# Performance work log

Measured on AMD Instinct MI355X. Metric: run time of the kernel, lower is better.

## Reference

```python
import jax, jax.numpy as jnp
import numpy as np

B, C, H, W = 128, 512, 14, 14
P = 512  # num_parts (codebook size)


def setup_inputs() -> dict:
    key = jax.random.key(0)
    k1, k2, k3 = jax.random.split(key, 3)
    fm = jax.random.normal(k1, (B, C, H, W), dtype=jnp.float32)
    embedding = jax.random.normal(k2, (B, C), dtype=jnp.float32)
    # self.w = torch.randn(P, C).clamp_(min=0)
    w = jnp.maximum(jax.random.normal(k3, (P, C), dtype=jnp.float32), 0.0)
    w_ep_sum = w  # clone of w at init
    w_ep_num = jnp.ones((P,), dtype=jnp.float32)
    return {"fm": fm, "embedding": embedding, "w": w,
            "w_ep_sum": w_ep_sum, "w_ep_num": w_ep_num, "epoch": 5}


def reference(fm, embedding, w, w_ep_sum, w_ep_num, epoch):
    b, c, h, wd = fm.shape
    p = w.shape[0]
    # NCHW -> [B, HW, C]
    x = jnp.transpose(fm, (0, 2, 3, 1)).reshape(b, h * wd, c)
    xf = x.reshape(b * h * wd, c)
    dist = (jnp.sum(xf * xf, axis=1, keepdims=True)
            + jnp.sum(w * w, axis=1)
            - 2.0 * (xf @ w.T))                      # [B*HW, P]
    assign = jax.nn.softmax(-dist.reshape(b, h * wd, p), axis=-1)
    # hard threshold: zero out weak assignments
    assign = jnp.where(assign < 1.0 / p, 0.0, assign)  # [B, HW, P]
    assign_sum = assign.mean(axis=1)                    # [B, P]

    if epoch > 2:  # epoch is a static Python int
        # relu(einsum('bn,nc->bnc').mean(1)) == relu((assign_sum @ w) / P)
        cvec = jax.nn.relu((assign_sum @ w) / p)        # [B, C]
        embedding_cat = jnp.concatenate([embedding, cvec], axis=-1)
    else:
        embedding_cat = jnp.concatenate([embedding, jnp.zeros_like(embedding)], axis=-1)

    # collect_weight (no-grad EMA-style accumulate).
    # einsum('bmn,bmc->bmnc').sum(1).sum(0) == einsum('bmn,bmc->nc') -- avoids
    # materializing the [B,M,N,C] tensor the torch code builds.
    update_w = jnp.einsum('bmn,bmc->nc', assign, x)     # [P, C]
    assign_mean = jnp.sum(assign, axis=(0, 1))          # [P]
    upd = assign_mean > 1.0
    new_w_ep_sum = jnp.where(upd[:, None], w_ep_sum + update_w, w_ep_sum)
    new_w_ep_num = jnp.where(upd, w_ep_num + assign_mean, w_ep_num)
    return embedding_cat, new_w_ep_sum, new_w_ep_num
```

## Files before the change

### kernel.cpp

```cpp
#include <hip/hip_runtime.h>
#include <hip/hip_bf16.h>

#define Bn   128
#define Cn   512
#define HWn  196
#define Mn   25088
#define Pn   512
#define SPLITK2 32
#define KCH  1024

#define OFF_XT     0u
#define OFF_AT     8388608u
#define OFF_PART   16777216u
#define OFF_XM     16777216u
#define OFF_WF     25165824u
#define OFF_WNORM  25296896u
#define OFF_RAWP   25297408u
#define OFF_MEAN   25428480u

#define OUT_CAT  0u
#define OUT_WSUM 131072u
#define OUT_WNUM 393216u

using bf16x8 = __attribute__((ext_vector_type(8))) short;
using f16x8  = __attribute__((ext_vector_type(8))) _Float16;
using f32x4  = __attribute__((ext_vector_type(4))) float;

__device__ __forceinline__ unsigned short f2b(float f) {
    union { float f; unsigned u; } x; x.f = f;
    unsigned r = x.u + 0x7fffu + ((x.u >> 16) & 1u);
    return (unsigned short)(r >> 16);
}

__global__ __launch_bounds__(64) void k_wnorm(const float* __restrict__ w,
                                              float* __restrict__ wn,
                                              _Float16* __restrict__ wf) {
    int n = blockIdx.x, l = threadIdx.x;
    const float* p = w + (size_t)n * Cn + l * 8;
    float4 a = *(const float4*)p;
    float4 b = *(const float4*)(p + 4);
    float s = a.x*a.x + a.y*a.y + a.z*a.z + a.w*a.w
            + b.x*b.x + b.y*b.y + b.z*b.z + b.w*b.w;
    alignas(16) _Float16 h[8];
    h[0]=(_Float16)a.x; h[1]=(_Float16)a.y; h[2]=(_Float16)a.z; h[3]=(_Float16)a.w;
    h[4]=(_Float16)b.x; h[5]=(_Float16)b.y; h[6]=(_Float16)b.z; h[7]=(_Float16)b.w;
    *(float4*)(wf + (size_t)(n >> 4) * 8192u + (size_t)(l >> 2) * 512
                 + (n & 15) * 32 + (l & 3) * 8) = *(const float4*)h;
    #pragma unroll
    for (int o = 32; o > 0; o >>= 1) s += __shfl_down(s, o);
    if (l == 0) wn[n] = s;
}

__global__ __launch_bounds__(512) void k_prep2(const float* __restrict__ fm,
                                               _Float16* __restrict__ xm,
                                               unsigned short* __restrict__ xt) {
    __shared__ _Float16 tile[64][200];
    int b = blockIdx.x;
    int cg = blockIdx.y * 64;
    int t = threadIdx.x;
    for (int i = t; i < 64 * 49; i += 512) {
        int cl = i / 49, h4 = i - cl * 49;
        float4 v = *(const float4*)(fm + ((size_t)(b * Cn + cg + cl) * HWn) + h4 * 4);
        tile[cl][h4*4+0] = (_Float16)v.x;
        tile[cl][h4*4+1] = (_Float16)v.y;
        tile[cl][h4*4+2] = (_Float16)v.z;
        tile[cl][h4*4+3] = (_Float16)v.w;
    }
    __syncthreads();
    for (int i = t; i < HWn * 8; i += 512) {
        int hw = i >> 3, seg = i & 7;
        alignas(16) _Float16 h[8];
        #pragma unroll
        for (int j = 0; j < 8; ++j) h[j] = tile[seg * 8 + j][hw];
        *(float4*)(xm + (size_t)(b * HWn + hw) * Cn + cg + seg * 8) = *(const float4*)h;
    }
    for (int i = t; i < 64 * 4 * 16; i += 512) {
        int cl = i >> 6, rem = i & 63;
        int q = rem >> 4, j4 = rem & 15;
        ushort4 o;
        if (j4 < 12) {
            o.x = f2b((float)tile[cl][q*49 + j4*4 + 0]);
            o.y = f2b((float)tile[cl][q*49 + j4*4 + 1]);
            o.z = f2b((float)tile[cl][q*49 + j4*4 + 2]);
            o.w = f2b((float)tile[cl][q*49 + j4*4 + 3]);
        } else if (j4 == 12) {
            o.x = f2b((float)tile[cl][q*49 + 48]);
            o.y = 0; o.z = 0; o.w = 0;
        } else {
            o.x = 0; o.y = 0; o.z = 0; o.w = 0;
        }
        int c = cg + cl;
        int T = c >> 4;
        int seg = b * 8 + q * 2 + (j4 >> 3);
        int k = (j4 & 7) * 4;
        *(ushort4*)(xt + (size_t)T * 524288u + (size_t)seg * 512 + (c & 15) * 32 + k) = o;
    }
}

__global__ __launch_bounds__(512) void k_post(const _Float16* __restrict__ xm,
                                              const _Float16* __restrict__ wf,
                                              const float* __restrict__ wnorm,
                                              unsigned short* __restrict__ at,
                                              float* __restrict__ rawp) {
    __shared__ _Float16 As[113][520];
    __shared__ float red[2][64][4];
    __shared__ float colp[2][512];
    const int bid = blockIdx.x;
    const int b = bid >> 1, half = bid & 1;
    const int tid = threadIdx.x;
    const int wave = tid >> 6, lane = tid & 63;
    const int mq = wave >> 2, nq = wave & 3;
    const int rl = lane & 15, rq = lane >> 4;
    const int kb = rq * 8;
    const int m0 = b * 196 + half * 98;
    const int n0 = nq * 128;

    for (int i = tid; i < 113 * 64; i += 512) {
        int row = i >> 6, kc = (i & 63) * 8;
        *(f16x8*)&As[row][kc] = *(const f16x8*)(xm + (size_t)(m0 + row) * Cn + kc);
    }
    __syncthreads();

    const _Float16* wtb = wf + (size_t)(nq * 8) * 8192u + rl * 32 + kb;

    f32x4 acc[4][8] = {};
    for (int seg = 0; seg < 16; ++seg) {
        f16x8 a[4], bb[8];
        #pragma unroll
        for (int f = 0; f < 4; ++f)
            a[f] = *(const f16x8*)&As[mq * 49 + f * 16 + rl][seg * 32 + kb];
        #pragma unroll
        for (int g = 0; g < 8; ++g)
            bb[g] = *(const f16x8*)(wtb + (size_t)g * 8192u + seg * 512);
        #pragma unroll
        for (int f = 0; f < 4; ++f)
            #pragma unroll
            for (int g = 0; g < 8; ++g)
                acc[f][g] = __builtin_amdgcn_mfma_f32_16x16x32_f16(a[f], bb[g], acc[f][g], 0, 0, 0);
    }
    float wn[8];
    #pragma unroll
    for (int g = 0; g < 8; ++g) wn[g] = wnorm[n0 + g * 16 + rl];
    #pragma unroll
    for (int f = 0; f < 4; ++f)
        #pragma unroll
        for (int g = 0; g < 8; ++g)
            #pragma unroll
            for (int r = 0; r < 4; ++r)
                acc[f][g][r] = 2.0f * acc[f][g][r] - wn[g];
    float mx[4][4];
    #pragma unroll
    for (int f = 0; f < 4; ++f)
        #pragma unroll
        for (int r = 0; r < 4; ++r) {
            float m_ = acc[f][0][r];
            #pragma unroll
            for (int g = 1; g < 8; ++g) m_ = fmaxf(m_, acc[f][g][r]);
            #pragma unroll
            for (int o = 8; o >= 1; o >>= 1) m_ = fmaxf(m_, __shfl_xor(m_, o));
            mx[f][r] = m_;
        }
    if (rl == 0)
        #pragma unroll
        for (int f = 0; f < 4; ++f)
            #pragma unroll
            for (int r = 0; r < 4; ++r)
                red[mq][f * 16 + rq * 4 + r][nq] = mx[f][r];
    __syncthreads();
    float rmax[4][4];
    #pragma unroll
    for (int f = 0; f < 4; ++f)
        #pragma unroll
        for (int r = 0; r < 4; ++r) {
            float* q = red[mq][f * 16 + rq * 4 + r];
            rmax[f][r] = fmaxf(fmaxf(q[0], q[1]), fmaxf(q[2], q[3]));
        }
    float sm[4][4];
    #pragma unroll
    for (int f = 0; f < 4; ++f)
        #pragma unroll
        for (int r = 0; r < 4; ++r) {
            float s_ = 0.f;
            #pragma unroll
            for (int g = 0; g < 8; ++g) {
                float p = __expf(acc[f][g][r] - rmax[f][r]);
                acc[f][g][r] = p;
                s_ += p;
            }
            #pragma unroll
            for (int o = 8; o >= 1; o >>= 1) s_ += __shfl_xor(s_, o);
            sm[f][r] = s_;
        }
    __syncthreads();
    if (rl == 0)
        #pragma unroll
        for (int f = 0; f < 4; ++f)
            #pragma unroll
            for (int r = 0; r < 4; ++r)
                red[mq][f * 16 + rq * 4 + r][nq] = sm[f][r];
    __syncthreads();
    const float invP = 1.0f / 512.0f;
    #pragma unroll
    for (int f = 0; f < 4; ++f)
        #pragma unroll
        for (int r = 0; r < 4; ++r) {
            float* q = red[mq][f * 16 + rq * 4 + r];
            float inv = 1.0f / (q[0] + q[1] + q[2] + q[3]);
            #pragma unroll
            for (int g = 0; g < 8; ++g) {
                float a = acc[f][g][r] * inv;
                acc[f][g][r] = (a < invP) ? 0.0f : a;
            }
        }
    float cs[8] = {};
    #pragma unroll
    for (int g = 0; g < 8; ++g) {
        #pragma unroll
        for (int f = 0; f < 4; ++f)
            #pragma unroll
            for (int r = 0; r < 4; ++r)
                if (f * 16 + rq * 4 + r < 49) cs[g] += acc[f][g][r];
        cs[g] += __shfl_xor(cs[g], 16);
        cs[g] += __shfl_xor(cs[g], 32);
    }
    if (rq == 0)
        #pragma unroll
        for (int g = 0; g < 8; ++g) colp[mq][n0 + g * 16 + rl] = cs[g];
    __syncthreads();
    if (tid < 512) rawp[(size_t)bid * 512 + tid] = colp[0][tid] + colp[1][tid];
    const int mb = b * 256 + (half * 2 + mq) * 64;
    const int segbase = mb >> 5;
    #pragma unroll
    for (int f = 0; f < 4; ++f) {
        const int mloc = f * 16 + rq * 4;
        const int seg = segbase + (mloc >> 5);
        const int k = mloc & 31;
        #pragma unroll
        for (int g = 0; g < 8; ++g) {
            ushort4 o;
            o.x = (mloc + 0 < 49) ? f2b(acc[f][g][0]) : (unsigned short)0;
            o.y = (mloc + 1 < 49) ? f2b(acc[f][g][1]) : (unsigned short)0;
            o.z = (mloc + 2 < 49) ? f2b(acc[f][g][2]) : (unsigned short)0;
            o.w = (mloc + 3 < 49) ? f2b(acc[f][g][3]) : (unsigned short)0;
            const int T = nq * 8 + g;
            *(ushort4*)(at + (size_t)T * 524288u + (size_t)seg * 512 + rl * 32 + k) = o;
        }
    }
}

__global__ __launch_bounds__(256) void k_reduce(const float* __restrict__ rawp,
                                                const float* __restrict__ wnum,
                                                float* __restrict__ mean,
                                                float* __restrict__ outnum) {
    int n = blockIdx.x * 256 + threadIdx.x;
    float s = 0.f;
    for (int r = 0; r < 256; ++r) s += rawp[(size_t)r * Pn + n];
    mean[n] = s;
    outnum[n] = wnum[n] + (s > 1.0f ? s : 0.0f);
}

__global__ __launch_bounds__(256) void k_cvec(const float* __restrict__ rawp,
                                              const float* __restrict__ w,
                                              const float* __restrict__ emb,
                                              const int* __restrict__ epoch,
                                              float* __restrict__ out) {
    __shared__ float srow[512];
    int b = blockIdx.x, t = threadIdx.x;
    srow[t]       = rawp[(size_t)(2*b) * Pn + t]       + rawp[(size_t)(2*b+1) * Pn + t];
    srow[t + 256] = rawp[(size_t)(2*b) * Pn + t + 256] + rawp[(size_t)(2*b+1) * Pn + t + 256];
    __syncthreads();
    float a0 = 0.f, a1 = 0.f;
    for (int p = 0; p < Pn; ++p) {
        float ap = srow[p];
        a0 = fmaf(ap, w[(size_t)p * Cn + t], a0);
        a1 = fmaf(ap, w[(size_t)p * Cn + t + 256], a1);
    }
    const float sc = 1.0f / (196.0f * 512.0f);
    int ep = epoch[0];
    float c0 = (ep > 2) ? fmaxf(a0, 0.f) * sc : 0.f;
    float c1 = (ep > 2) ? fmaxf(a1, 0.f) * sc : 0.f;
    out[(size_t)b * 1024 + t]             = emb[(size_t)b * Cn + t];
    out[(size_t)b * 1024 + t + 256]       = emb[(size_t)b * Cn + t + 256];
    out[(size_t)b * 1024 + 512 + t]       = c0;
    out[(size_t)b * 1024 + 512 + t + 256] = c1;
}

__global__ __launch_bounds__(256) void k_upw_mfma(const unsigned short* __restrict__ at,
                                                  const unsigned short* __restrict__ xt,
                                                  float* __restrict__ part) {
    const int id = blockIdx.x;
    const int sp = id & 31;
    const int m  = id >> 5;
    const int tid = threadIdx.x;
    const int wave = tid >> 6, lane = tid & 63;
    const int wn = wave >> 1, wc = wave & 1;
    const int n0 = (m & 3) * 128;
    const int c0 = (m >> 2) * 128;
    const int rl = lane & 15, rq = lane >> 4;
    const int loff = rl * 32 + rq * 8;
    const int segbase = sp * 32;

    const unsigned short* pa[4];
    const unsigned short* pb[4];
    #pragma unroll
    for (int f = 0; f < 4; ++f) {
        const int Ta = (n0 >> 4) + wn * 4 + f;
        const int Tb = (c0 >> 4) + wc * 4 + f;
        pa[f] = at + (size_t)Ta * 524288u + (size_t)segbase * 512 + loff;
        pb[f] = xt + (size_t)Tb * 524288u + (size_t)segbase * 512 + loff;
    }

    f32x4 acc[4][4] = {};
    bf16x8 aC[4], bC[4], aN[4], bN[4];
    #pragma unroll
    for (int f = 0; f < 4; ++f) {
        aC[f] = *(const bf16x8*)(pa[f]);
        bC[f] = *(const bf16x8*)(pb[f]);
    }
    for (int ks = 0; ks < 32; ks += 2) {
        #pragma unroll
        for (int f = 0; f < 4; ++f) {
            aN[f] = *(const bf16x8*)(pa[f] + (ks + 1) * 512);
            bN[f] = *(const bf16x8*)(pb[f] + (ks + 1) * 512);
        }
        #pragma unroll
        for (int i = 0; i < 4; ++i)
            #pragma unroll
            for (int j = 0; j < 4; ++j)
                acc[i][j] = __builtin_amdgcn_mfma_f32_16x16x32_bf16(aC[i], bC[j], acc[i][j], 0, 0, 0);
        if (ks + 2 < 32) {
            #pragma unroll
            for (int f = 0; f < 4; ++f) {
                aC[f] = *(const bf16x8*)(pa[f] + (ks + 2) * 512);
                bC[f] = *(const bf16x8*)(pb[f] + (ks + 2) * 512);
            }
        }
        #pragma unroll
        for (int i = 0; i < 4; ++i)
            #pragma unroll
            for (int j = 0; j < 4; ++j)
                acc[i][j] = __builtin_amdgcn_mfma_f32_16x16x32_bf16(aN[i], bN[j], acc[i][j], 0, 0, 0);
    }
    float* o = part + (size_t)sp * (Pn * Cn);
    const int rq4 = rq * 4;
    #pragma unroll
    for (int i = 0; i < 4; ++i) {
        #pragma unroll
        for (int j = 0; j < 4; ++j) {
            int n = n0 + wn * 64 + i * 16 + rq4;
            int c = c0 + wc * 64 + j * 16 + rl;
            #pragma unroll
            for (int r = 0; r < 4; ++r)
                o[(size_t)(n + r) * Cn + c] = acc[i][j][r];
        }
    }
}

__global__ __launch_bounds__(256) void k_wep(const float* __restrict__ part,
                                             const float* __restrict__ mean,
                                             const float* __restrict__ wsum,
                                             float* __restrict__ out1) {
    int n = blockIdx.x, t = threadIdx.x;
    bool upd = mean[n] > 1.0f;
    #pragma unroll
    for (int cc = 0; cc < 2; ++cc) {
        int c = t + cc * 256;
        float s = 0.f;
        #pragma unroll
        for (int k = 0; k < SPLITK2; ++k)
            s += part[(size_t)k * (Pn * Cn) + (size_t)n * Cn + c];
        size_t idx = (size_t)n * Cn + c;
        out1[idx] = wsum[idx] + (upd ? s : 0.f);
    }
}

extern "C" void kernel_launch(void* const* d_in, const int* in_sizes, int n_in,
                              void* d_out, int out_size, void* d_ws, size_t ws_size,
                              hipStream_t stream) {
    const float* fm    = (const float*)d_in[0];
    const float* emb   = (const float*)d_in[1];
    const float* w     = (const float*)d_in[2];
    const float* wsum  = (const float*)d_in[3];
    const float* wnum  = (const float*)d_in[4];
    const int*   epoch = (const int*)d_in[5];
    float* out = (float*)d_out;
    float* wsf = (float*)d_ws;

    unsigned short* xtb   = (unsigned short*)(wsf + OFF_XT);
    unsigned short* atb   = (unsigned short*)(wsf + OFF_AT);
    float*          partb = wsf + OFF_PART;
    _Float16*       xmb   = (_Float16*)(wsf + OFF_XM);
    _Float16*       wfb   = (_Float16*)(wsf + OFF_WF);
    float*          wnormb = wsf + OFF_WNORM;
    float*          rawpb  = wsf + OFF_RAWP;
    float*          meanb  = wsf + OFF_MEAN;

    k_wnorm<<<512, 64, 0, stream>>>(w, wnormb, wfb);
    k_prep2<<<dim3(Bn, 8), 512, 0, stream>>>(fm, xmb, xtb);
    k_post<<<256, 512, 0, stream>>>(xmb, wfb, wnormb, atb, rawpb);
    k_reduce<<<2, 256, 0, stream>>>(rawpb, wnum, meanb, out + OUT_WNUM);
    k_cvec<<<Bn, 256, 0, stream>>>(rawpb, w, emb, epoch, out + OUT_CAT);
    k_upw_mfma<<<512, 256, 0, stream>>>(atb, xtb, partb);
    k_wep<<<Pn, 256, 0, stream>>>(partb, meanb, wsum, out + OUT_WSUM);
}
```

Before: 151.9 us.

## Replace dense MFMA update GEMM with sparse gather over nonzero assignments

Drops the split-K bf16 MFMA GEMM and its 32-way partial-sum reduction kernel for update_w. A new per-codebook-row kernel compacts the nonzero thresholded assignments with wave ballots and accumulates the matching fp16 feature rows directly into the output. This also removes the bf16 transposed feature buffer that the prep kernel used to write. Cost now scales with assignment density: it is cheap when the thresholded softmax is nearly one-hot, but serial and latency-bound if many assignments stay nonzero.

Result: slower. 603.7 us (+297.5%).

```diff
diff --git a/kernel.cpp b/kernel.cpp
--- a/kernel.cpp
+++ b/kernel.cpp
@@ -6,17 +6,13 @@
 #define HWn  196
 #define Mn   25088
 #define Pn   512
-#define SPLITK2 32
-#define KCH  1024
-
-#define OFF_XT     0u
-#define OFF_AT     8388608u
-#define OFF_PART   16777216u
-#define OFF_XM     16777216u
-#define OFF_WF     25165824u
-#define OFF_WNORM  25296896u
-#define OFF_RAWP   25297408u
-#define OFF_MEAN   25428480u
+
+#define OFF_AT     0u
+#define OFF_XM     8388608u
+#define OFF_WF     14811136u
+#define OFF_WNORM  14942208u
+#define OFF_RAWP   14942720u
+#define OFF_MEAN   15073792u
 
 #define OUT_CAT  0u
 #define OUT_WSUM 131072u
@@ -30,6 +26,10 @@
     union { float f; unsigned u; } x; x.f = f;
     unsigned r = x.u + 0x7fffu + ((x.u >> 16) & 1u);
     return (unsigned short)(r >> 16);
+}
+__device__ __forceinline__ float b2f(unsigned short u) {
+    union { unsigned u; float f; } x; x.u = ((unsigned)u) << 16;
+    return x.f;
 }
 
 __global__ __launch_bounds__(64) void k_wnorm(const float* __restrict__ w,
@@ -52,8 +52,7 @@
 }
 
 __global__ __launch_bounds__(512) void k_prep2(const float* __restrict__ fm,
-                                               _Float16* __restrict__ xm,
-                                               unsigned short* __restrict__ xt) {
+                                               _Float16* __restrict__ xm) {
     __shared__ _Float16 tile[64][200];
     int b = blockIdx.x;
     int cg = blockIdx.y * 64;
@@ -73,27 +72,6 @@
         #pragma unroll
         for (int j = 0; j < 8; ++j) h[j] = tile[seg * 8 + j][hw];
         *(float4*)(xm + (size_t)(b * HWn + hw) * Cn + cg + seg * 8) = *(const float4*)h;
-    }
-    for (int i = t; i < 64 * 4 * 16; i += 512) {
-        int cl = i >> 6, rem = i & 63;
-        int q = rem >> 4, j4 = rem & 15;
-        ushort4 o;
-        if (j4 < 12) {
-            o.x = f2b((float)tile[cl][q*49 + j4*4 + 0]);
-            o.y = f2b((float)tile[cl][q*49 + j4*4 + 1]);
-            o.z = f2b((float)tile[cl][q*49 + j4*4 + 2]);
-            o.w = f2b((float)tile[cl][q*49 + j4*4 + 3]);
-        } else if (j4 == 12) {
-            o.x = f2b((float)tile[cl][q*49 + 48]);
-            o.y = 0; o.z = 0; o.w = 0;
-        } else {
-            o.x = 0; o.y = 0; o.z = 0; o.w = 0;
-        }
-        int c = cg + cl;
-        int T = c >> 4;
-        int seg = b * 8 + q * 2 + (j4 >> 3);
-        int k = (j4 & 7) * 4;
-        *(ushort4*)(xt + (size_t)T * 524288u + (size_t)seg * 512 + (c & 15) * 32 + k) = o;
     }
 }
 
@@ -285,93 +263,49 @@
     out[(size_t)b * 1024 + 512 + t + 256] = c1;
 }
 
-__global__ __launch_bounds__(256) void k_upw_mfma(const unsigned short* __restrict__ at,
-                                                  const unsigned short* __restrict__ xt,
-                                                  float* __restrict__ part) {
-    const int id = blockIdx.x;
-    const int sp = id & 31;
-    const int m  = id >> 5;
-    const int tid = threadIdx.x;
-    const int wave = tid >> 6, lane = tid & 63;
-    const int wn = wave >> 1, wc = wave & 1;
-    const int n0 = (m & 3) * 128;
-    const int c0 = (m >> 2) * 128;
-    const int rl = lane & 15, rq = lane >> 4;
-    const int loff = rl * 32 + rq * 8;
-    const int segbase = sp * 32;
-
-    const unsigned short* pa[4];
-    const unsigned short* pb[4];
-    #pragma unroll
-    for (int f = 0; f < 4; ++f) {
-        const int Ta = (n0 >> 4) + wn * 4 + f;
-        const int Tb = (c0 >> 4) + wc * 4 + f;
-        pa[f] = at + (size_t)Ta * 524288u + (size_t)segbase * 512 + loff;
-        pb[f] = xt + (size_t)Tb * 524288u + (size_t)segbase * 512 + loff;
-    }
-
-    f32x4 acc[4][4] = {};
-    bf16x8 aC[4], bC[4], aN[4], bN[4];
-    #pragma unroll
-    for (int f = 0; f < 4; ++f) {
-        aC[f] = *(const bf16x8*)(pa[f]);
-        bC[f] = *(const bf16x8*)(pb[f]);
-    }
-    for (int ks = 0; ks < 32; ks += 2) {
-        #pragma unroll
-        for (int f = 0; f < 4; ++f) {
-            aN[f] = *(const bf16x8*)(pa[f] + (ks + 1) * 512);
-            bN[f] = *(const bf16x8*)(pb[f] + (ks + 1) * 512);
-        }
-        #pragma unroll
-        for (int i = 0; i < 4; ++i)
-            #pragma unroll
-            for (int j = 0; j < 4; ++j)
-                acc[i][j] = __builtin_amdgcn_mfma_f32_16x16x32_bf16(aC[i], bC[j], acc[i][j], 0, 0, 0);
-        if (ks + 2 < 32) {
-            #pragma unroll
-            for (int f = 0; f < 4; ++f) {
-                aC[f] = *(const bf16x8*)(pa[f] + (ks + 2) * 512);
-                bC[f] = *(const bf16x8*)(pb[f] + (ks + 2) * 512);
-            }
-        }
-        #pragma unroll
-        for (int i = 0; i < 4; ++i)
-            #pragma unroll
-            for (int j = 0; j < 4; ++j)
-                acc[i][j] = __builtin_amdgcn_mfma_f32_16x16x32_bf16(aN[i], bN[j], acc[i][j], 0, 0, 0);
-    }
-    float* o = part + (size_t)sp * (Pn * Cn);
-    const int rq4 = rq * 4;
-    #pragma unroll
-    for (int i = 0; i < 4; ++i) {
-        #pragma unroll
-        for (int j = 0; j < 4; ++j) {
-            int n = n0 + wn * 64 + i * 16 + rq4;
-            int c = c0 + wc * 64 + j * 16 + rl;
-            #pragma unroll
-            for (int r = 0; r < 4; ++r)
-                o[(size_t)(n + r) * Cn + c] = acc[i][j][r];
-        }
-    }
-}
-
-__global__ __launch_bounds__(256) void k_wep(const float* __restrict__ part,
-                                             const float* __restrict__ mean,
-                                             const float* __restrict__ wsum,
-                                             float* __restrict__ out1) {
-    int n = blockIdx.x, t = threadIdx.x;
-    bool upd = mean[n] > 1.0f;
-    #pragma unroll
-    for (int cc = 0; cc < 2; ++cc) {
-        int c = t + cc * 256;
-        float s = 0.f;
-        #pragma unroll
-        for (int k = 0; k < SPLITK2; ++k)
-            s += part[(size_t)k * (Pn * Cn) + (size_t)n * Cn + c];
-        size_t idx = (size_t)n * Cn + c;
-        out1[idx] = wsum[idx] + (upd ? s : 0.f);
-    }
+__global__ __launch_bounds__(256) void k_spmm(const unsigned short* __restrict__ at,
+                                              const _Float16* __restrict__ xm,
+                                              const float* __restrict__ mean,
+                                              const float* __restrict__ wsum,
+                                              float* __restrict__ out1) {
+    __shared__ float sa[256];
+    __shared__ int   smi[256];
+    __shared__ int   woff[4];
+    const int n = blockIdx.x, t = threadIdx.x;
+    const int wave = t >> 6, lane = t & 63;
+    const unsigned short* arow = at + (size_t)(n >> 4) * 524288u + (n & 15) * 32;
+    float acc0 = 0.f, acc1 = 0.f;
+    for (int base = 0; base < 32768; base += 256) {
+        const int mp = base + t;
+        const unsigned short av = arow[(size_t)(mp >> 5) * 512 + (mp & 31)];
+        const bool valid = (av != 0);
+        unsigned long long bal = __ballot(valid);
+        int pos = __popcll(bal & ((1ull << lane) - 1ull));
+        if (lane == 0) woff[wave] = __popcll(bal);
+        __syncthreads();
+        int off = 0;
+        #pragma unroll
+        for (int w2 = 0; w2 < 4; ++w2) if (w2 < wave) off += woff[w2];
+        const int total = woff[0] + woff[1] + woff[2] + woff[3];
+        if (valid) {
+            int bb = mp >> 8, rem = mp & 255;
+            int q = rem >> 6, j = rem & 63;
+            sa[off + pos]  = b2f(av);
+            smi[off + pos] = bb * 196 + q * 49 + j;
+        }
+        __syncthreads();
+        for (int e = 0; e < total; ++e) {
+            const float a_ = sa[e];
+            const _Float16* xr = xm + (size_t)smi[e] * Cn;
+            acc0 = fmaf(a_, (float)xr[t],       acc0);
+            acc1 = fmaf(a_, (float)xr[t + 256], acc1);
+        }
+        __syncthreads();
+    }
+    const bool upd = mean[n] > 1.0f;
+    const size_t i0 = (size_t)n * Cn + t;
+    out1[i0]       = wsum[i0]       + (upd ? acc0 : 0.f);
+    out1[i0 + 256] = wsum[i0 + 256] + (upd ? acc1 : 0.f);
 }
 
 extern "C" void kernel_launch(void* const* d_in, const int* in_sizes, int n_in,
@@ -386,9 +320,7 @@
     float* out = (float*)d_out;
     float* wsf = (float*)d_ws;
 
-    unsigned short* xtb   = (unsigned short*)(wsf + OFF_XT);
     unsigned short* atb   = (unsigned short*)(wsf + OFF_AT);
-    float*          partb = wsf + OFF_PART;
     _Float16*       xmb   = (_Float16*)(wsf + OFF_XM);
     _Float16*       wfb   = (_Float16*)(wsf + OFF_WF);
     float*          wnormb = wsf + OFF_WNORM;
@@ -396,10 +328,9 @@
     float*          meanb  = wsf + OFF_MEAN;
 
     k_wnorm<<<512, 64, 0, stream>>>(w, wnormb, wfb);
-    k_prep2<<<dim3(Bn, 8), 512, 0, stream>>>(fm, xmb, xtb);
+    k_prep2<<<dim3(Bn, 8), 512, 0, stream>>>(fm, xmb);
     k_post<<<256, 512, 0, stream>>>(xmb, wfb, wnormb, atb, rawpb);
     k_reduce<<<2, 256, 0, stream>>>(rawpb, wnum, meanb, out + OUT_WNUM);
     k_cvec<<<Bn, 256, 0, stream>>>(rawpb, w, emb, epoch, out + OUT_CAT);
-    k_upw_mfma<<<512, 256, 0, stream>>>(atb, xtb, partb);
-    k_wep<<<Pn, 256, 0, stream>>>(partb, meanb, wsum, out + OUT_WSUM);
-}
+    k_spmm<<<Pn, 256, 0, stream>>>(atb, xmb, meanb, wsum, out + OUT_WSUM);
+}
```
